# Optimization experiments

Hardware: AMD Instinct MI355X
Metric: run time of the kernel (lower is better)

## Reference

```python
import jax, jax.numpy as jnp
import numpy as np

B, N, F_IN, T_IN = 64, 307, 3, 12
HID = 128


def setup_inputs() -> dict:
    key = jax.random.key(0)
    ks = jax.random.split(key, 7)
    s = 1.0 / np.sqrt(HID)
    x = jax.random.normal(ks[0], (B, N, F_IN, T_IN), dtype=jnp.float32)
    W_ih = jax.random.uniform(ks[1], (4 * HID, F_IN), minval=-s, maxval=s, dtype=jnp.float32)
    W_hh = jax.random.uniform(ks[2], (4 * HID, HID), minval=-s, maxval=s, dtype=jnp.float32)
    b_ih = jax.random.uniform(ks[3], (4 * HID,), minval=-s, maxval=s, dtype=jnp.float32)
    b_hh = jax.random.uniform(ks[4], (4 * HID,), minval=-s, maxval=s, dtype=jnp.float32)
    W_lin = jax.random.uniform(ks[5], (1, HID), minval=-s, maxval=s, dtype=jnp.float32)
    b_lin = jax.random.uniform(ks[6], (1,), minval=-s, maxval=s, dtype=jnp.float32)
    return {"x": x, "W_ih": W_ih, "W_hh": W_hh, "b_ih": b_ih, "b_hh": b_hh, "W_lin": W_lin, "b_lin": b_lin}


def _lstm_forward(x, W_ih, W_hh, b_ih, b_hh, W_lin, b_lin):
    # x: (B, N, F_in, T_in) -> permute -> (B, N, T, F) -> reshape (B*N, T, F)
    xp = jnp.transpose(x, (0, 1, 3, 2)).reshape(B * N, T_IN, F_IN)
    # PyTorch nn.LSTM default batch_first=False: dim0 (B*N) is the time axis,
    # dim1 (T_IN) is the batch axis. We faithfully scan over B*N steps.
    # Precompute input gates for all steps: (S, Tb, 4H)
    gx = jnp.einsum('stf,gf->stg', xp, W_ih) + b_ih + b_hh
    W_hh_T = W_hh.T  # (H, 4H)

    def step(carry, g):
        h, c = carry  # (Tb, H)
        z = g + h @ W_hh_T  # (Tb, 4H)
        i, f, gg, o = jnp.split(z, 4, axis=-1)
        c = jax.nn.sigmoid(f) * c + jax.nn.sigmoid(i) * jnp.tanh(gg)
        h = jax.nn.sigmoid(o) * jnp.tanh(c)
        return (h, c), h

    h0 = jnp.zeros((T_IN, HID), dtype=x.dtype)
    _, hs = jax.lax.scan(step, (h0, h0), gx)  # hs: (S, Tb, H)
    out = hs @ W_lin.T + b_lin  # (S, Tb, 1)
    return out.reshape(B, N, T_IN)


def reference(x, W_ih, W_hh, b_ih, b_hh, W_lin, b_lin):
    return _lstm_forward(x, W_ih, W_hh, b_ih, b_hh, W_lin, b_lin)
```

## Files before the change

### kernel.cpp

```cpp
#include <hip/hip_runtime.h>

#define S_TOTAL 19648
#define T_CH    12
#define HID     128
#define NT      512

#define CHUNK_L 77
#define NCHUNK  256
#define WARMUP  32

typedef _Float16 half8  __attribute__((ext_vector_type(8)));
typedef _Float16 half4v __attribute__((ext_vector_type(4)));
typedef _Float16 half2v __attribute__((ext_vector_type(2)));
typedef float f4 __attribute__((ext_vector_type(4)));

#define NLOG2E  (-1.4426950408889634f)
#define N2LOG2E (-2.8853900817779268f)

#if __has_builtin(__builtin_amdgcn_exp2f)
#define EXP2(x) __builtin_amdgcn_exp2f(x)
#else
#define EXP2(x) __expf((x) * 0.69314718055994531f)
#endif

__device__ __forceinline__ float sigz(float z) {
    return __builtin_amdgcn_rcpf(1.0f + EXP2(z));
}
__device__ __forceinline__ float tanz(float z) {
    return __builtin_fmaf(2.0f, __builtin_amdgcn_rcpf(1.0f + EXP2(z)), -1.0f);
}
__device__ __forceinline__ float fdot2(half2v a, half2v b, float c) {
    return __builtin_amdgcn_fdot2(a, b, c, false);
}
#define MFMA(A, B, C) __builtin_amdgcn_mfma_f32_16x16x32_f16(A, B, C, 0, 0, 0)

__global__ __launch_bounds__(NT, 2) void lstm_fused(
    const float* __restrict__ x,
    const float* __restrict__ W_ih,
    const float* __restrict__ W_hh,
    const float* __restrict__ b_ih,
    const float* __restrict__ b_hh,
    const float* __restrict__ W_lin,
    const float* __restrict__ b_lin,
    float* __restrict__ out)
{
    const int tid = threadIdx.x;
    const int w   = tid >> 6;
    const int l   = tid & 63;
    const int n   = l & 15;
    const int qk  = l >> 4;

    const int ostart = blockIdx.x * CHUNK_L;
    const int oend   = min(ostart + CHUNK_L, S_TOTAL);
    const int sbeg   = max(0, ostart - WARMUP);
    const int nsteps = oend - sbeg;

    __shared__ __align__(16) _Float16 hfrag[2][5][64][8];
    __shared__ float pout[2][16][8];

    half8 A[4][5];
#pragma unroll
    for (int q = 0; q < 4; ++q) {
        const float sc = (q == 2) ? N2LOG2E : NLOG2E;
        const int row = q * HID + 16 * w + (l & 15);
#pragma unroll
        for (int kt = 0; kt < 4; ++kt) {
            const float* src = &W_hh[row * HID + kt * 32 + qk * 8];
            half8 a;
#pragma unroll
            for (int e = 0; e < 8; ++e) a[e] = (_Float16)(src[e] * sc);
            A[q][kt] = a;
        }
        half8 ae = {};
        if (qk == 0) {
            ae[0] = (_Float16)(W_ih[row * 3 + 0] * sc);
            ae[1] = (_Float16)(W_ih[row * 3 + 1] * sc);
            ae[2] = (_Float16)(W_ih[row * 3 + 2] * sc);
            ae[3] = (_Float16)((b_ih[row] + b_hh[row]) * sc);
        }
        A[q][4] = ae;
    }

    const int j0 = 16 * w + 4 * qk;
    half2v wl01, wl23;
    wl01[0] = (_Float16)W_lin[j0];     wl01[1] = (_Float16)W_lin[j0 + 1];
    wl23[0] = (_Float16)W_lin[j0 + 2]; wl23[1] = (_Float16)W_lin[j0 + 3];
    const float blin = b_lin[0];

    ((uint4*)hfrag)[tid] = make_uint4(0, 0, 0, 0);
    if (tid < 128) ((uint4*)hfrag)[512 + tid] = make_uint4(0, 0, 0, 0);
    __syncthreads();
    if (tid < 16) {
        hfrag[0][4][tid][3] = (_Float16)1.0f;
        hfrag[1][4][tid][3] = (_Float16)1.0f;
    }
    if (tid < T_CH) {
        hfrag[0][4][tid][0] = (_Float16)x[sbeg * 36 + tid];
        hfrag[0][4][tid][1] = (_Float16)x[sbeg * 36 + 12 + tid];
        hfrag[0][4][tid][2] = (_Float16)x[sbeg * 36 + 24 + tid];
    }

    const _Float16* rb0 = &hfrag[0][0][l][0];
    const _Float16* rb1 = &hfrag[1][0][l][0];
    const int ktw = w >> 1;
    const int lp  = (2 * (w & 1) + (qk >> 1)) * 16 + n;
    _Float16* wb0 = &hfrag[0][ktw][lp][4 * (qk & 1)];
    _Float16* wb1 = &hfrag[1][ktw][lp][4 * (qk & 1)];

    float c0 = 0.f, c1 = 0.f, c2 = 0.f, c3 = 0.f;

    float xn1a = 0.f, xn1b = 0.f, xn1c = 0.f;
    float xn2a = 0.f, xn2b = 0.f, xn2c = 0.f;
    if (w == 0 && l < T_CH) {
        const int s1 = min(sbeg + 1, S_TOTAL - 1);
        const int s2 = min(sbeg + 2, S_TOTAL - 1);
        xn1a = x[s1 * 36 + l]; xn1b = x[s1 * 36 + 12 + l]; xn1c = x[s1 * 36 + 24 + l];
        xn2a = x[s2 * 36 + l]; xn2b = x[s2 * 36 + 12 + l]; xn2c = x[s2 * 36 + 24 + l];
    }
    __syncthreads();

    auto step = [&](const int p, const int s) {
        const _Float16* rb = p ? rb1 : rb0;

        const half8 B0 = *(const half8*)(rb + 0 * 512);
        const half8 B1 = *(const half8*)(rb + 1 * 512);
        const half8 B2 = *(const half8*)(rb + 2 * 512);
        const half8 B3 = *(const half8*)(rb + 3 * 512);
        const half8 B4 = *(const half8*)(rb + 4 * 512);

        if (w == 7 && l < T_CH && s > ostart) {
            const f4 pa = *(const f4*)&pout[p ^ 1][l][0];
            const f4 pb = *(const f4*)&pout[p ^ 1][l][4];
            out[(s - 1) * T_CH + l] =
                pa.x + pa.y + pa.z + pa.w + pb.x + pb.y + pb.z + pb.w + blin;
        }
        if (w == 0 && l < T_CH) {
            _Float16* xd = p ? &hfrag[0][4][l][0] : &hfrag[1][4][l][0];
            half2v xp; xp[0] = (_Float16)xn1a; xp[1] = (_Float16)xn1b;
            *(half2v*)xd = xp;
            xd[2] = (_Float16)xn1c;
            xn1a = xn2a; xn1b = xn2b; xn1c = xn2c;
            const int sn = min(s + 3, S_TOTAL - 1);
            xn2a = x[sn * 36 + l];
            xn2b = x[sn * 36 + 12 + l];
            xn2c = x[sn * 36 + 24 + l];
        }

        const f4 z = {0.f, 0.f, 0.f, 0.f};
        f4 a0A = MFMA(A[0][4], B4, z), a1A = MFMA(A[1][4], B4, z);
        f4 a2A = MFMA(A[2][4], B4, z), a3A = MFMA(A[3][4], B4, z);
        f4 a0B = MFMA(A[0][2], B2, z), a1B = MFMA(A[1][2], B2, z);
        f4 a2B = MFMA(A[2][2], B2, z), a3B = MFMA(A[3][2], B2, z);
        a0A = MFMA(A[0][0], B0, a0A); a1A = MFMA(A[1][0], B0, a1A);
        a2A = MFMA(A[2][0], B0, a2A); a3A = MFMA(A[3][0], B0, a3A);
        a0B = MFMA(A[0][3], B3, a0B); a1B = MFMA(A[1][3], B3, a1B);
        a2B = MFMA(A[2][3], B3, a2B); a3B = MFMA(A[3][3], B3, a3B);
        a0A = MFMA(A[0][1], B1, a0A); a1A = MFMA(A[1][1], B1, a1A);
        a2A = MFMA(A[2][1], B1, a2A); a3A = MFMA(A[3][1], B1, a3A);
        const f4 ac0 = a0A + a0B, ac1 = a1A + a1B;
        const f4 ac2 = a2A + a2B, ac3 = a3A + a3B;

        float h0, h1, h2, h3;
        {
            const float i0 = sigz(ac0[0]), f0 = sigz(ac1[0]);
            const float g0 = tanz(ac2[0]), o0 = sigz(ac3[0]);
            c0 = __builtin_fmaf(f0, c0, i0 * g0);  h0 = o0 * tanz(c0 * N2LOG2E);
            const float i1 = sigz(ac0[1]), f1 = sigz(ac1[1]);
            const float g1 = tanz(ac2[1]), o1 = sigz(ac3[1]);
            c1 = __builtin_fmaf(f1, c1, i1 * g1);  h1 = o1 * tanz(c1 * N2LOG2E);
            const float i2 = sigz(ac0[2]), f2 = sigz(ac1[2]);
            const float g2 = tanz(ac2[2]), o2 = sigz(ac3[2]);
            c2 = __builtin_fmaf(f2, c2, i2 * g2);  h2 = o2 * tanz(c2 * N2LOG2E);
            const float i3 = sigz(ac0[3]), f3 = sigz(ac1[3]);
            const float g3 = tanz(ac2[3]), o3 = sigz(ac3[3]);
            c3 = __builtin_fmaf(f3, c3, i3 * g3);  h3 = o3 * tanz(c3 * N2LOG2E);
        }

        half4v hv;
        hv[0] = (_Float16)h0; hv[1] = (_Float16)h1;
        hv[2] = (_Float16)h2; hv[3] = (_Float16)h3;
        *(half4v*)(p ? wb0 : wb1) = hv;

        if (s >= ostart) {
            half2v hp01, hp23;
            hp01[0] = hv[0]; hp01[1] = hv[1];
            hp23[0] = hv[2]; hp23[1] = hv[3];
            float pp = fdot2(hp23, wl23, fdot2(hp01, wl01, 0.0f));
            pp += __shfl_xor(pp, 16, 64);
            pp += __shfl_xor(pp, 32, 64);
            if (qk == 0) pout[p][n][w] = pp;
        }
        __syncthreads();
    };

    int ss = 0;
    for (; ss + 2 <= nsteps; ss += 2) {
        step(0, sbeg + ss);
        step(1, sbeg + ss + 1);
    }
    if (ss < nsteps) step(0, sbeg + ss);

    if (w == 7 && l < T_CH) {
        const int pf = (nsteps - 1) & 1;
        const f4 pa = *(const f4*)&pout[pf][l][0];
        const f4 pb = *(const f4*)&pout[pf][l][4];
        out[(oend - 1) * T_CH + l] =
            pa.x + pa.y + pa.z + pa.w + pb.x + pb.y + pb.z + pb.w + blin;
    }
}

extern "C" void kernel_launch(void* const* d_in, const int* in_sizes, int n_in,
                              void* d_out, int out_size, void* d_ws, size_t ws_size,
                              hipStream_t stream) {
    const float* x     = (const float*)d_in[0];
    const float* W_ih  = (const float*)d_in[1];
    const float* W_hh  = (const float*)d_in[2];
    const float* b_ih  = (const float*)d_in[3];
    const float* b_hh  = (const float*)d_in[4];
    const float* W_lin = (const float*)d_in[5];
    const float* b_lin = (const float*)d_in[6];
    float* out = (float*)d_out;

    hipLaunchKernelGGL(lstm_fused, dim3(NCHUNK), dim3(NT), 0, stream,
                       x, W_ih, W_hh, b_ih, b_hh, W_lin, b_lin, out);
}
```

Measured before the change: 179.6 us.

## Interleave two independent sequence chunks per block to hide recurrence latency

Each block now runs two independent time chunks (A and B) of half the previous length side by side, issuing their MFMAs interleaved and sharing one barrier per step. This targets the serial dependency latency of the per-step recurrence: the B chain can fill MFMA and transcendental pipeline bubbles while the A chain waits. Halving the chunk length shortens the serial critical path, but the fixed 32-step warmup now covers a larger share of each chunk, so redundant work rises and per-thread register and LDS use roughly doubles.

```diff
diff --git a/kernel.cpp b/kernel.cpp
--- a/kernel.cpp
+++ b/kernel.cpp
@@ -5,8 +5,8 @@
 #define HID     128
 #define NT      512
 
-#define CHUNK_L 77
-#define NCHUNK  256
+#define CHUNK_L 39
+#define NBLK    252
 #define WARMUP  32
 
 typedef _Float16 half8  __attribute__((ext_vector_type(8)));
@@ -50,13 +50,17 @@
     const int n   = l & 15;
     const int qk  = l >> 4;
 
-    const int ostart = blockIdx.x * CHUNK_L;
-    const int oend   = min(ostart + CHUNK_L, S_TOTAL);
-    const int sbeg   = max(0, ostart - WARMUP);
-    const int nsteps = oend - sbeg;
-
-    __shared__ __align__(16) _Float16 hfrag[2][5][64][8];
-    __shared__ float pout[2][16][8];
+    const int cA = 2 * blockIdx.x, cB = cA + 1;
+    const int ostartA = cA * CHUNK_L, oendA = min(ostartA + CHUNK_L, S_TOTAL);
+    const int ostartB = cB * CHUNK_L, oendB = min(ostartB + CHUNK_L, S_TOTAL);
+    const int sbegA = max(0, ostartA - WARMUP);
+    const int sbegB = max(0, ostartB - WARMUP);
+    const int nstepsA = oendA - sbegA;
+    const int nstepsB = oendB - sbegB;
+    const int nsteps  = max(nstepsA, nstepsB);
+
+    __shared__ __align__(16) _Float16 hfrag[2][2][5][64][8];
+    __shared__ __align__(16) float pout[2][2][16][8];
 
     half8 A[4][5];
 #pragma unroll
@@ -87,124 +91,211 @@
     wl23[0] = (_Float16)W_lin[j0 + 2]; wl23[1] = (_Float16)W_lin[j0 + 3];
     const float blin = b_lin[0];
 
-    ((uint4*)hfrag)[tid] = make_uint4(0, 0, 0, 0);
-    if (tid < 128) ((uint4*)hfrag)[512 + tid] = make_uint4(0, 0, 0, 0);
+    uint4* hz = (uint4*)hfrag;
+    hz[tid]       = make_uint4(0, 0, 0, 0);
+    hz[tid + 512] = make_uint4(0, 0, 0, 0);
+    if (tid < 256) hz[tid + 1024] = make_uint4(0, 0, 0, 0);
     __syncthreads();
     if (tid < 16) {
-        hfrag[0][4][tid][3] = (_Float16)1.0f;
-        hfrag[1][4][tid][3] = (_Float16)1.0f;
-    }
-    if (tid < T_CH) {
-        hfrag[0][4][tid][0] = (_Float16)x[sbeg * 36 + tid];
-        hfrag[0][4][tid][1] = (_Float16)x[sbeg * 36 + 12 + tid];
-        hfrag[0][4][tid][2] = (_Float16)x[sbeg * 36 + 24 + tid];
-    }
-
-    const _Float16* rb0 = &hfrag[0][0][l][0];
-    const _Float16* rb1 = &hfrag[1][0][l][0];
+        hfrag[0][0][4][tid][3] = (_Float16)1.0f;
+        hfrag[0][1][4][tid][3] = (_Float16)1.0f;
+        hfrag[1][0][4][tid][3] = (_Float16)1.0f;
+        hfrag[1][1][4][tid][3] = (_Float16)1.0f;
+    }
+    if (w == 0 && l < T_CH) {
+        hfrag[0][0][4][l][0] = (_Float16)x[sbegA * 36 + l];
+        hfrag[0][0][4][l][1] = (_Float16)x[sbegA * 36 + 12 + l];
+        hfrag[0][0][4][l][2] = (_Float16)x[sbegA * 36 + 24 + l];
+    }
+    if (w == 1 && l < T_CH) {
+        hfrag[1][0][4][l][0] = (_Float16)x[sbegB * 36 + l];
+        hfrag[1][0][4][l][1] = (_Float16)x[sbegB * 36 + 12 + l];
+        hfrag[1][0][4][l][2] = (_Float16)x[sbegB * 36 + 24 + l];
+    }
+
+    const _Float16* rbA0 = &hfrag[0][0][0][l][0];
+    const _Float16* rbA1 = &hfrag[0][1][0][l][0];
+    const _Float16* rbB0 = &hfrag[1][0][0][l][0];
+    const _Float16* rbB1 = &hfrag[1][1][0][l][0];
     const int ktw = w >> 1;
     const int lp  = (2 * (w & 1) + (qk >> 1)) * 16 + n;
-    _Float16* wb0 = &hfrag[0][ktw][lp][4 * (qk & 1)];
-    _Float16* wb1 = &hfrag[1][ktw][lp][4 * (qk & 1)];
-
-    float c0 = 0.f, c1 = 0.f, c2 = 0.f, c3 = 0.f;
-
-    float xn1a = 0.f, xn1b = 0.f, xn1c = 0.f;
-    float xn2a = 0.f, xn2b = 0.f, xn2c = 0.f;
+    _Float16* wbA0 = &hfrag[0][0][ktw][lp][4 * (qk & 1)];
+    _Float16* wbA1 = &hfrag[0][1][ktw][lp][4 * (qk & 1)];
+    _Float16* wbB0 = &hfrag[1][0][ktw][lp][4 * (qk & 1)];
+    _Float16* wbB1 = &hfrag[1][1][ktw][lp][4 * (qk & 1)];
+
+    float cA0 = 0.f, cA1 = 0.f, cA2 = 0.f, cA3 = 0.f;
+    float cB0 = 0.f, cB1 = 0.f, cB2 = 0.f, cB3 = 0.f;
+
+    float xA1a = 0.f, xA1b = 0.f, xA1c = 0.f, xA2a = 0.f, xA2b = 0.f, xA2c = 0.f;
+    float xB1a = 0.f, xB1b = 0.f, xB1c = 0.f, xB2a = 0.f, xB2b = 0.f, xB2c = 0.f;
     if (w == 0 && l < T_CH) {
-        const int s1 = min(sbeg + 1, S_TOTAL - 1);
-        const int s2 = min(sbeg + 2, S_TOTAL - 1);
-        xn1a = x[s1 * 36 + l]; xn1b = x[s1 * 36 + 12 + l]; xn1c = x[s1 * 36 + 24 + l];
-        xn2a = x[s2 * 36 + l]; xn2b = x[s2 * 36 + 12 + l]; xn2c = x[s2 * 36 + 24 + l];
+        const int s1 = min(sbegA + 1, S_TOTAL - 1);
+        const int s2 = min(sbegA + 2, S_TOTAL - 1);
+        xA1a = x[s1 * 36 + l]; xA1b = x[s1 * 36 + 12 + l]; xA1c = x[s1 * 36 + 24 + l];
+        xA2a = x[s2 * 36 + l]; xA2b = x[s2 * 36 + 12 + l]; xA2c = x[s2 * 36 + 24 + l];
+    }
+    if (w == 1 && l < T_CH) {
+        const int s1 = min(sbegB + 1, S_TOTAL - 1);
+        const int s2 = min(sbegB + 2, S_TOTAL - 1);
+        xB1a = x[s1 * 36 + l]; xB1b = x[s1 * 36 + 12 + l]; xB1c = x[s1 * 36 + 24 + l];
+        xB2a = x[s2 * 36 + l]; xB2b = x[s2 * 36 + 12 + l]; xB2c = x[s2 * 36 + 24 + l];
     }
     __syncthreads();
 
-    auto step = [&](const int p, const int s) {
-        const _Float16* rb = p ? rb1 : rb0;
-
-        const half8 B0 = *(const half8*)(rb + 0 * 512);
-        const half8 B1 = *(const half8*)(rb + 1 * 512);
-        const half8 B2 = *(const half8*)(rb + 2 * 512);
-        const half8 B3 = *(const half8*)(rb + 3 * 512);
-        const half8 B4 = *(const half8*)(rb + 4 * 512);
-
-        if (w == 7 && l < T_CH && s > ostart) {
-            const f4 pa = *(const f4*)&pout[p ^ 1][l][0];
-            const f4 pb = *(const f4*)&pout[p ^ 1][l][4];
-            out[(s - 1) * T_CH + l] =
+    auto step = [&](const int p, const int sA, const int sB) {
+        const _Float16* ra = p ? rbA1 : rbA0;
+        const _Float16* rb = p ? rbB1 : rbB0;
+
+        const half8 BA0 = *(const half8*)(ra + 0 * 512);
+        const half8 BA1 = *(const half8*)(ra + 1 * 512);
+        const half8 BA2 = *(const half8*)(ra + 2 * 512);
+        const half8 BA3 = *(const half8*)(ra + 3 * 512);
+        const half8 BA4 = *(const half8*)(ra + 4 * 512);
+        const half8 BB0 = *(const half8*)(rb + 0 * 512);
+        const half8 BB1 = *(const half8*)(rb + 1 * 512);
+        const half8 BB2 = *(const half8*)(rb + 2 * 512);
+        const half8 BB3 = *(const half8*)(rb + 3 * 512);
+        const half8 BB4 = *(const half8*)(rb + 4 * 512);
+
+        if (w == 7 && l < T_CH && sA > ostartA && sA <= oendA) {
+            const f4 pa = *(const f4*)&pout[0][p ^ 1][l][0];
+            const f4 pb = *(const f4*)&pout[0][p ^ 1][l][4];
+            out[(sA - 1) * T_CH + l] =
                 pa.x + pa.y + pa.z + pa.w + pb.x + pb.y + pb.z + pb.w + blin;
         }
+        if (w == 6 && l < T_CH && sB > ostartB && sB <= oendB) {
+            const f4 pa = *(const f4*)&pout[1][p ^ 1][l][0];
+            const f4 pb = *(const f4*)&pout[1][p ^ 1][l][4];
+            out[(sB - 1) * T_CH + l] =
+                pa.x + pa.y + pa.z + pa.w + pb.x + pb.y + pb.z + pb.w + blin;
+        }
+
         if (w == 0 && l < T_CH) {
-            _Float16* xd = p ? &hfrag[0][4][l][0] : &hfrag[1][4][l][0];
-            half2v xp; xp[0] = (_Float16)xn1a; xp[1] = (_Float16)xn1b;
+            _Float16* xd = p ? &hfrag[0][0][4][l][0] : &hfrag[0][1][4][l][0];
+            half2v xp; xp[0] = (_Float16)xA1a; xp[1] = (_Float16)xA1b;
             *(half2v*)xd = xp;
-            xd[2] = (_Float16)xn1c;
-            xn1a = xn2a; xn1b = xn2b; xn1c = xn2c;
-            const int sn = min(s + 3, S_TOTAL - 1);
-            xn2a = x[sn * 36 + l];
-            xn2b = x[sn * 36 + 12 + l];
-            xn2c = x[sn * 36 + 24 + l];
+            xd[2] = (_Float16)xA1c;
+            xA1a = xA2a; xA1b = xA2b; xA1c = xA2c;
+            const int sn = min(sA + 3, S_TOTAL - 1);
+            xA2a = x[sn * 36 + l];
+            xA2b = x[sn * 36 + 12 + l];
+            xA2c = x[sn * 36 + 24 + l];
+        }
+        if (w == 1 && l < T_CH) {
+            _Float16* xd = p ? &hfrag[1][0][4][l][0] : &hfrag[1][1][4][l][0];
+            half2v xp; xp[0] = (_Float16)xB1a; xp[1] = (_Float16)xB1b;
+            *(half2v*)xd = xp;
+            xd[2] = (_Float16)xB1c;
+            xB1a = xB2a; xB1b = xB2b; xB1c = xB2c;
+            const int sn = min(sB + 3, S_TOTAL - 1);
+            xB2a = x[sn * 36 + l];
+            xB2b = x[sn * 36 + 12 + l];
+            xB2c = x[sn * 36 + 24 + l];
         }
 
         const f4 z = {0.f, 0.f, 0.f, 0.f};
-        f4 a0A = MFMA(A[0][4], B4, z), a1A = MFMA(A[1][4], B4, z);
-        f4 a2A = MFMA(A[2][4], B4, z), a3A = MFMA(A[3][4], B4, z);
-        f4 a0B = MFMA(A[0][2], B2, z), a1B = MFMA(A[1][2], B2, z);
-        f4 a2B = MFMA(A[2][2], B2, z), a3B = MFMA(A[3][2], B2, z);
-        a0A = MFMA(A[0][0], B0, a0A); a1A = MFMA(A[1][0], B0, a1A);
-        a2A = MFMA(A[2][0], B0, a2A); a3A = MFMA(A[3][0], B0, a3A);
-        a0B = MFMA(A[0][3], B3, a0B); a1B = MFMA(A[1][3], B3, a1B);
-        a2B = MFMA(A[2][3], B3, a2B); a3B = MFMA(A[3][3], B3, a3B);
-        a0A = MFMA(A[0][1], B1, a0A); a1A = MFMA(A[1][1], B1, a1A);
-        a2A = MFMA(A[2][1], B1, a2A); a3A = MFMA(A[3][1], B1, a3A);
-        const f4 ac0 = a0A + a0B, ac1 = a1A + a1B;
-        const f4 ac2 = a2A + a2B, ac3 = a3A + a3B;
-
-        float h0, h1, h2, h3;
+        f4 aA0 = MFMA(A[0][4], BA4, z), aB0 = MFMA(A[0][4], BB4, z);
+        f4 aA1 = MFMA(A[1][4], BA4, z), aB1 = MFMA(A[1][4], BB4, z);
+        f4 aA2 = MFMA(A[2][4], BA4, z), aB2 = MFMA(A[2][4], BB4, z);
+        f4 aA3 = MFMA(A[3][4], BA4, z), aB3 = MFMA(A[3][4], BB4, z);
+        aA0 = MFMA(A[0][0], BA0, aA0); aB0 = MFMA(A[0][0], BB0, aB0);
+        aA1 = MFMA(A[1][0], BA0, aA1); aB1 = MFMA(A[1][0], BB0, aB1);
+        aA2 = MFMA(A[2][0], BA0, aA2); aB2 = MFMA(A[2][0], BB0, aB2);
+        aA3 = MFMA(A[3][0], BA0, aA3); aB3 = MFMA(A[3][0], BB0, aB3);
+        aA0 = MFMA(A[0][1], BA1, aA0); aB0 = MFMA(A[0][1], BB1, aB0);
+        aA1 = MFMA(A[1][1], BA1, aA1); aB1 = MFMA(A[1][1], BB1, aB1);
+        aA2 = MFMA(A[2][1], BA1, aA2); aB2 = MFMA(A[2][1], BB1, aB2);
+        aA3 = MFMA(A[3][1], BA1, aA3); aB3 = MFMA(A[3][1], BB1, aB3);
+        aA0 = MFMA(A[0][2], BA2, aA0); aB0 = MFMA(A[0][2], BB2, aB0);
+        aA1 = MFMA(A[1][2], BA2, aA1); aB1 = MFMA(A[1][2], BB2, aB1);
+        aA2 = MFMA(A[2][2], BA2, aA2); aB2 = MFMA(A[2][2], BB2, aB2);
+        aA3 = MFMA(A[3][2], BA2, aA3); aB3 = MFMA(A[3][2], BB2, aB3);
+        aA0 = MFMA(A[0][3], BA3, aA0); aB0 = MFMA(A[0][3], BB3, aB0);
+        aA1 = MFMA(A[1][3], BA3, aA1); aB1 = MFMA(A[1][3], BB3, aB1);
+        aA2 = MFMA(A[2][3], BA3, aA2); aB2 = MFMA(A[2][3], BB3, aB2);
+        aA3 = MFMA(A[3][3], BA3, aA3); aB3 = MFMA(A[3][3], BB3, aB3);
+
+        float hA0, hA1, hA2, hA3;
         {
-            const float i0 = sigz(ac0[0]), f0 = sigz(ac1[0]);
-            const float g0 = tanz(ac2[0]), o0 = sigz(ac3[0]);
-            c0 = __builtin_fmaf(f0, c0, i0 * g0);  h0 = o0 * tanz(c0 * N2LOG2E);
-            const float i1 = sigz(ac0[1]), f1 = sigz(ac1[1]);
-            const float g1 = tanz(ac2[1]), o1 = sigz(ac3[1]);
-            c1 = __builtin_fmaf(f1, c1, i1 * g1);  h1 = o1 * tanz(c1 * N2LOG2E);
-            const float i2 = sigz(ac0[2]), f2 = sigz(ac1[2]);
-            const float g2 = tanz(ac2[2]), o2 = sigz(ac3[2]);
-            c2 = __builtin_fmaf(f2, c2, i2 * g2);  h2 = o2 * tanz(c2 * N2LOG2E);
-            const float i3 = sigz(ac0[3]), f3 = sigz(ac1[3]);
-            const float g3 = tanz(ac2[3]), o3 = sigz(ac3[3]);
-            c3 = __builtin_fmaf(f3, c3, i3 * g3);  h3 = o3 * tanz(c3 * N2LOG2E);
-        }
-
-        half4v hv;
-        hv[0] = (_Float16)h0; hv[1] = (_Float16)h1;
-        hv[2] = (_Float16)h2; hv[3] = (_Float16)h3;
-        *(half4v*)(p ? wb0 : wb1) = hv;
-
-        if (s >= ostart) {
-            half2v hp01, hp23;
-            hp01[0] = hv[0]; hp01[1] = hv[1];
-            hp23[0] = hv[2]; hp23[1] = hv[3];
-            float pp = fdot2(hp23, wl23, fdot2(hp01, wl01, 0.0f));
+            const float i0 = sigz(aA0[0]), f0 = sigz(aA1[0]);
+            const float g0 = tanz(aA2[0]), o0 = sigz(aA3[0]);
+            cA0 = __builtin_fmaf(f0, cA0, i0 * g0);  hA0 = o0 * tanz(cA0 * N2LOG2E);
+            const float i1 = sigz(aA0[1]), f1 = sigz(aA1[1]);
+            const float g1 = tanz(aA2[1]), o1 = sigz(aA3[1]);
+            cA1 = __builtin_fmaf(f1, cA1, i1 * g1);  hA1 = o1 * tanz(cA1 * N2LOG2E);
+            const float i2 = sigz(aA0[2]), f2 = sigz(aA1[2]);
+            const float g2 = tanz(aA2[2]), o2 = sigz(aA3[2]);
+            cA2 = __builtin_fmaf(f2, cA2, i2 * g2);  hA2 = o2 * tanz(cA2 * N2LOG2E);
+            const float i3 = sigz(aA0[3]), f3 = sigz(aA1[3]);
+            const float g3 = tanz(aA2[3]), o3 = sigz(aA3[3]);
+            cA3 = __builtin_fmaf(f3, cA3, i3 * g3);  hA3 = o3 * tanz(cA3 * N2LOG2E);
+        }
+        half4v hvA;
+        hvA[0] = (_Float16)hA0; hvA[1] = (_Float16)hA1;
+        hvA[2] = (_Float16)hA2; hvA[3] = (_Float16)hA3;
+        *(half4v*)(p ? wbA0 : wbA1) = hvA;
+
+        float hB0, hB1, hB2, hB3;
+        {
+            const float i0 = sigz(aB0[0]), f0 = sigz(aB1[0]);
+            const float g0 = tanz(aB2[0]), o0 = sigz(aB3[0]);
+            cB0 = __builtin_fmaf(f0, cB0, i0 * g0);  hB0 = o0 * tanz(cB0 * N2LOG2E);
+            const float i1 = sigz(aB0[1]), f1 = sigz(aB1[1]);
+            const float g1 = tanz(aB2[1]), o1 = sigz(aB3[1]);
+            cB1 = __builtin_fmaf(f1, cB1, i1 * g1);  hB1 = o1 * tanz(cB1 * N2LOG2E);
+            const float i2 = sigz(aB0[2]), f2 = sigz(aB1[2]);
+            const float g2 = tanz(aB2[2]), o2 = sigz(aB3[2]);
+            cB2 = __builtin_fmaf(f2, cB2, i2 * g2);  hB2 = o2 * tanz(cB2 * N2LOG2E);
+            const float i3 = sigz(aB0[3]), f3 = sigz(aB1[3]);
+            const float g3 = tanz(aB2[3]), o3 = sigz(aB3[3]);
+            cB3 = __builtin_fmaf(f3, cB3, i3 * g3);  hB3 = o3 * tanz(cB3 * N2LOG2E);
+        }
+        half4v hvB;
+        hvB[0] = (_Float16)hB0; hvB[1] = (_Float16)hB1;
+        hvB[2] = (_Float16)hB2; hvB[3] = (_Float16)hB3;
+        *(half4v*)(p ? wbB0 : wbB1) = hvB;
+
+        if (sA >= ostartA && sA < oendA) {
+            half2v h01, h23;
+            h01[0] = hvA[0]; h01[1] = hvA[1];
+            h23[0] = hvA[2]; h23[1] = hvA[3];
+            float pp = fdot2(h23, wl23, fdot2(h01, wl01, 0.0f));
             pp += __shfl_xor(pp, 16, 64);
             pp += __shfl_xor(pp, 32, 64);
-            if (qk == 0) pout[p][n][w] = pp;
+            if (qk == 0) pout[0][p][n][w] = pp;
+        }
+        if (sB >= ostartB && sB < oendB) {
+            half2v h01, h23;
+            h01[0] = hvB[0]; h01[1] = hvB[1];
+            h23[0] = hvB[2]; h23[1] = hvB[3];
+            float pp = fdot2(h23, wl23, fdot2(h01, wl01, 0.0f));
+            pp += __shfl_xor(pp, 16, 64);
+            pp += __shfl_xor(pp, 32, 64);
+            if (qk == 0) pout[1][p][n][w] = pp;
         }
         __syncthreads();
     };
 
     int ss = 0;
     for (; ss + 2 <= nsteps; ss += 2) {
-        step(0, sbeg + ss);
-        step(1, sbeg + ss + 1);
-    }
-    if (ss < nsteps) step(0, sbeg + ss);
-
-    if (w == 7 && l < T_CH) {
+        step(0, sbegA + ss, sbegB + ss);
+        step(1, sbegA + ss + 1, sbegB + ss + 1);
+    }
+    if (ss < nsteps) step(0, sbegA + ss, sbegB + ss);
+
+    if (w == 7 && l < T_CH && nstepsA == nsteps) {
         const int pf = (nsteps - 1) & 1;
-        const f4 pa = *(const f4*)&pout[pf][l][0];
-        const f4 pb = *(const f4*)&pout[pf][l][4];
-        out[(oend - 1) * T_CH + l] =
+        const f4 pa = *(const f4*)&pout[0][pf][l][0];
+        const f4 pb = *(const f4*)&pout[0][pf][l][4];
+        out[(oendA - 1) * T_CH + l] =
+            pa.x + pa.y + pa.z + pa.w + pb.x + pb.y + pb.z + pb.w + blin;
+    }
+    if (w == 6 && l < T_CH && nstepsB == nsteps) {
+        const int pf = (nsteps - 1) & 1;
+        const f4 pa = *(const f4*)&pout[1][pf][l][0];
+        const f4 pb = *(const f4*)&pout[1][pf][l][4];
+        out[(oendB - 1) * T_CH + l] =
             pa.x + pa.y + pa.z + pa.w + pb.x + pb.y + pb.z + pb.w + blin;
     }
 }
@@ -221,6 +312,6 @@
     const float* b_lin = (const float*)d_in[6];
     float* out = (float*)d_out;
 
-    hipLaunchKernelGGL(lstm_fused, dim3(NCHUNK), dim3(NT), 0, stream,
+    hipLaunchKernelGGL(lstm_fused, dim3(NBLK), dim3(NT), 0, stream,
                        x, W_ih, W_hh, b_ih, b_hh, W_lin, b_lin, out);
 }
```

After: 193.9 us. 8.0% more time.

## Interleave two independent LSTM chunk chains per block to overlap MFMA and gate math

Applied to the files above, without the earlier changes.

Each block now runs two independent sequence chunks, halving the chunk length to 39 and launching 252 blocks. The loop alternates between them: one chain's recurrent MFMAs are issued while the other chain's gate nonlinearities, output reduction and input staging run, each in its own shared-memory buffer. This targets the latency-bound serial recurrence and cuts the number of serial steps per block. In exchange, the fixed 32-step warmup is now a larger share of each shorter chunk, and register pressure rises because two accumulator and cell-state sets are live at once.

```diff
diff --git a/kernel.cpp b/kernel.cpp
--- a/kernel.cpp
+++ b/kernel.cpp
@@ -5,8 +5,8 @@
 #define HID     128
 #define NT      512
 
-#define CHUNK_L 77
-#define NCHUNK  256
+#define CHUNK_L 39
+#define NBLK    252
 #define WARMUP  32
 
 typedef _Float16 half8  __attribute__((ext_vector_type(8)));
@@ -33,6 +33,95 @@
     return __builtin_amdgcn_fdot2(a, b, c, false);
 }
 #define MFMA(A, B, C) __builtin_amdgcn_mfma_f32_16x16x32_f16(A, B, C, 0, 0, 0)
+
+#define LOADS(CIDX)                                                      \
+    {                                                                    \
+        const _Float16* rbp = &hfrag[CIDX][0][l][0];                     \
+        Bf0 = *(const half8*)(rbp + 0 * 512);                            \
+        Bf1 = *(const half8*)(rbp + 1 * 512);                            \
+        Bf2 = *(const half8*)(rbp + 2 * 512);                            \
+        Bf3 = *(const half8*)(rbp + 3 * 512);                            \
+        Bf4 = *(const half8*)(rbp + 4 * 512);                            \
+    }
+
+#define MFMAS(X)                                                         \
+    {                                                                    \
+        const f4 z = {0.f, 0.f, 0.f, 0.f};                               \
+        a##X##0 = MFMA(A[0][4], Bf4, z);                                 \
+        a##X##1 = MFMA(A[1][4], Bf4, z);                                 \
+        a##X##2 = MFMA(A[2][4], Bf4, z);                                 \
+        a##X##3 = MFMA(A[3][4], Bf4, z);                                 \
+        a##X##0 = MFMA(A[0][0], Bf0, a##X##0);                           \
+        a##X##1 = MFMA(A[1][0], Bf0, a##X##1);                           \
+        a##X##2 = MFMA(A[2][0], Bf0, a##X##2);                           \
+        a##X##3 = MFMA(A[3][0], Bf0, a##X##3);                           \
+        a##X##0 = MFMA(A[0][1], Bf1, a##X##0);                           \
+        a##X##1 = MFMA(A[1][1], Bf1, a##X##1);                           \
+        a##X##2 = MFMA(A[2][1], Bf1, a##X##2);                           \
+        a##X##3 = MFMA(A[3][1], Bf1, a##X##3);                           \
+        a##X##0 = MFMA(A[0][2], Bf2, a##X##0);                           \
+        a##X##1 = MFMA(A[1][2], Bf2, a##X##1);                           \
+        a##X##2 = MFMA(A[2][2], Bf2, a##X##2);                           \
+        a##X##3 = MFMA(A[3][2], Bf2, a##X##3);                           \
+        a##X##0 = MFMA(A[0][3], Bf3, a##X##0);                           \
+        a##X##1 = MFMA(A[1][3], Bf3, a##X##1);                           \
+        a##X##2 = MFMA(A[2][3], Bf3, a##X##2);                           \
+        a##X##3 = MFMA(A[3][3], Bf3, a##X##3);                           \
+    }
+
+#define GATES(X, CIDX, WOUT, WXP, jv)                                    \
+    {                                                                    \
+        const int sX = sbeg##X + (jv);                                   \
+        const int pj = (jv) & 1;                                         \
+        if (w == (WOUT) && l < T_CH && sX > ostart##X && sX <= oend##X) {\
+            const f4 pa = *(const f4*)&pout[CIDX][pj ^ 1][l][0];         \
+            const f4 pb = *(const f4*)&pout[CIDX][pj ^ 1][l][4];         \
+            out[(sX - 1) * T_CH + l] = pa.x + pa.y + pa.z + pa.w         \
+                + pb.x + pb.y + pb.z + pb.w + blin;                      \
+        }                                                                \
+        if (w == (WXP) && l < T_CH) {                                    \
+            _Float16* xd = &hfrag[CIDX][4][l][0];                        \
+            half2v xp; xp[0] = (_Float16)x##X##1a;                       \
+            xp[1] = (_Float16)x##X##1b;                                  \
+            *(half2v*)xd = xp;                                           \
+            xd[2] = (_Float16)x##X##1c;                                  \
+            x##X##1a = x##X##2a; x##X##1b = x##X##2b;                    \
+            x##X##1c = x##X##2c;                                         \
+            const int sn = min(sX + 3, S_TOTAL - 1);                     \
+            x##X##2a = x[sn * 36 + l];                                   \
+            x##X##2b = x[sn * 36 + 12 + l];                              \
+            x##X##2c = x[sn * 36 + 24 + l];                              \
+        }                                                                \
+        const float i0 = sigz(a##X##0[0]), f0 = sigz(a##X##1[0]);        \
+        const float g0 = tanz(a##X##2[0]), o0 = sigz(a##X##3[0]);        \
+        c##X##0 = __builtin_fmaf(f0, c##X##0, i0 * g0);                  \
+        const float h0 = o0 * tanz(c##X##0 * N2LOG2E);                   \
+        const float i1 = sigz(a##X##0[1]), f1 = sigz(a##X##1[1]);        \
+        const float g1 = tanz(a##X##2[1]), o1 = sigz(a##X##3[1]);        \
+        c##X##1 = __builtin_fmaf(f1, c##X##1, i1 * g1);                  \
+        const float h1 = o1 * tanz(c##X##1 * N2LOG2E);                   \
+        const float i2 = sigz(a##X##0[2]), f2 = sigz(a##X##1[2]);        \
+        const float g2 = tanz(a##X##2[2]), o2 = sigz(a##X##3[2]);        \
+        c##X##2 = __builtin_fmaf(f2, c##X##2, i2 * g2);                  \
+        const float h2 = o2 * tanz(c##X##2 * N2LOG2E);                   \
+        const float i3 = sigz(a##X##0[3]), f3 = sigz(a##X##1[3]);        \
+        const float g3 = tanz(a##X##2[3]), o3 = sigz(a##X##3[3]);        \
+        c##X##3 = __builtin_fmaf(f3, c##X##3, i3 * g3);                  \
+        const float h3 = o3 * tanz(c##X##3 * N2LOG2E);                   \
+        half4v hv;                                                       \
+        hv[0] = (_Float16)h0; hv[1] = (_Float16)h1;                      \
+        hv[2] = (_Float16)h2; hv[3] = (_Float16)h3;                      \
+        *(half4v*)wb##X = hv;                                            \
+        if (sX >= ostart##X && sX < oend##X) {                           \
+            half2v h01, h23;                                             \
+            h01[0] = hv[0]; h01[1] = hv[1];                              \
+            h23[0] = hv[2]; h23[1] = hv[3];                              \
+            float pp = fdot2(h23, wl23, fdot2(h01, wl01, 0.0f));         \
+            pp += __shfl_xor(pp, 16, 64);                                \
+            pp += __shfl_xor(pp, 32, 64);                                \
+            if (qk == 0) pout[CIDX][pj][n][w] = pp;                      \
+        }                                                                \
+    }
 
 __global__ __launch_bounds__(NT, 2) void lstm_fused(
     const float* __restrict__ x,
@@ -50,13 +139,17 @@
     const int n   = l & 15;
     const int qk  = l >> 4;
 
-    const int ostart = blockIdx.x * CHUNK_L;
-    const int oend   = min(ostart + CHUNK_L, S_TOTAL);
-    const int sbeg   = max(0, ostart - WARMUP);
-    const int nsteps = oend - sbeg;
+    const int cA = 2 * blockIdx.x, cB = cA + 1;
+    const int ostartA = cA * CHUNK_L, oendA = min(ostartA + CHUNK_L, S_TOTAL);
+    const int ostartB = cB * CHUNK_L, oendB = min(ostartB + CHUNK_L, S_TOTAL);
+    const int sbegA = max(0, ostartA - WARMUP);
+    const int sbegB = max(0, ostartB - WARMUP);
+    const int nstepsA = oendA - sbegA;
+    const int nstepsB = oendB - sbegB;
+    const int nsteps  = max(nstepsA, nstepsB);
 
     __shared__ __align__(16) _Float16 hfrag[2][5][64][8];
-    __shared__ float pout[2][16][8];
+    __shared__ __align__(16) float pout[2][2][16][8];
 
     half8 A[4][5];
 #pragma unroll
@@ -87,124 +180,87 @@
     wl23[0] = (_Float16)W_lin[j0 + 2]; wl23[1] = (_Float16)W_lin[j0 + 3];
     const float blin = b_lin[0];
 
-    ((uint4*)hfrag)[tid] = make_uint4(0, 0, 0, 0);
-    if (tid < 128) ((uint4*)hfrag)[512 + tid] = make_uint4(0, 0, 0, 0);
+    uint4* hz = (uint4*)hfrag;
+    hz[tid] = make_uint4(0, 0, 0, 0);
+    if (tid < 128) hz[512 + tid] = make_uint4(0, 0, 0, 0);
     __syncthreads();
     if (tid < 16) {
         hfrag[0][4][tid][3] = (_Float16)1.0f;
         hfrag[1][4][tid][3] = (_Float16)1.0f;
     }
-    if (tid < T_CH) {
-        hfrag[0][4][tid][0] = (_Float16)x[sbeg * 36 + tid];
-        hfrag[0][4][tid][1] = (_Float16)x[sbeg * 36 + 12 + tid];
-        hfrag[0][4][tid][2] = (_Float16)x[sbeg * 36 + 24 + tid];
-    }
-
-    const _Float16* rb0 = &hfrag[0][0][l][0];
-    const _Float16* rb1 = &hfrag[1][0][l][0];
+    if (w == 0 && l < T_CH) {
+        hfrag[0][4][l][0] = (_Float16)x[sbegA * 36 + l];
+        hfrag[0][4][l][1] = (_Float16)x[sbegA * 36 + 12 + l];
+        hfrag[0][4][l][2] = (_Float16)x[sbegA * 36 + 24 + l];
+    }
+    if (w == 1 && l < T_CH) {
+        hfrag[1][4][l][0] = (_Float16)x[sbegB * 36 + l];
+        hfrag[1][4][l][1] = (_Float16)x[sbegB * 36 + 12 + l];
+        hfrag[1][4][l][2] = (_Float16)x[sbegB * 36 + 24 + l];
+    }
+
     const int ktw = w >> 1;
     const int lp  = (2 * (w & 1) + (qk >> 1)) * 16 + n;
-    _Float16* wb0 = &hfrag[0][ktw][lp][4 * (qk & 1)];
-    _Float16* wb1 = &hfrag[1][ktw][lp][4 * (qk & 1)];
-
-    float c0 = 0.f, c1 = 0.f, c2 = 0.f, c3 = 0.f;
-
-    float xn1a = 0.f, xn1b = 0.f, xn1c = 0.f;
-    float xn2a = 0.f, xn2b = 0.f, xn2c = 0.f;
+    _Float16* wbA = &hfrag[0][ktw][lp][4 * (qk & 1)];
+    _Float16* wbB = &hfrag[1][ktw][lp][4 * (qk & 1)];
+
+    f4 aA0 = {0.f,0.f,0.f,0.f}, aA1 = aA0, aA2 = aA0, aA3 = aA0;
+    f4 aB0 = aA0, aB1 = aA0, aB2 = aA0, aB3 = aA0;
+    float cA0 = 0.f, cA1 = 0.f, cA2 = 0.f, cA3 = 0.f;
+    float cB0 = 0.f, cB1 = 0.f, cB2 = 0.f, cB3 = 0.f;
+
+    float xA1a = 0.f, xA1b = 0.f, xA1c = 0.f, xA2a = 0.f, xA2b = 0.f, xA2c = 0.f;
+    float xB1a = 0.f, xB1b = 0.f, xB1c = 0.f, xB2a = 0.f, xB2b = 0.f, xB2c = 0.f;
     if (w == 0 && l < T_CH) {
-        const int s1 = min(sbeg + 1, S_TOTAL - 1);
-        const int s2 = min(sbeg + 2, S_TOTAL - 1);
-        xn1a = x[s1 * 36 + l]; xn1b = x[s1 * 36 + 12 + l]; xn1c = x[s1 * 36 + 24 + l];
-        xn2a = x[s2 * 36 + l]; xn2b = x[s2 * 36 + 12 + l]; xn2c = x[s2 * 36 + 24 + l];
+        const int s1 = min(sbegA + 1, S_TOTAL - 1);
+        const int s2 = min(sbegA + 2, S_TOTAL - 1);
+        xA1a = x[s1 * 36 + l]; xA1b = x[s1 * 36 + 12 + l]; xA1c = x[s1 * 36 + 24 + l];
+        xA2a = x[s2 * 36 + l]; xA2b = x[s2 * 36 + 12 + l]; xA2c = x[s2 * 36 + 24 + l];
+    }
+    if (w == 1 && l < T_CH) {
+        const int s1 = min(sbegB + 1, S_TOTAL - 1);
+        const int s2 = min(sbegB + 2, S_TOTAL - 1);
+        xB1a = x[s1 * 36 + l]; xB1b = x[s1 * 36 + 12 + l]; xB1c = x[s1 * 36 + 24 + l];
+        xB2a = x[s2 * 36 + l]; xB2b = x[s2 * 36 + 12 + l]; xB2c = x[s2 * 36 + 24 + l];
     }
     __syncthreads();
 
-    auto step = [&](const int p, const int s) {
-        const _Float16* rb = p ? rb1 : rb0;
-
-        const half8 B0 = *(const half8*)(rb + 0 * 512);
-        const half8 B1 = *(const half8*)(rb + 1 * 512);
-        const half8 B2 = *(const half8*)(rb + 2 * 512);
-        const half8 B3 = *(const half8*)(rb + 3 * 512);
-        const half8 B4 = *(const half8*)(rb + 4 * 512);
-
-        if (w == 7 && l < T_CH && s > ostart) {
-            const f4 pa = *(const f4*)&pout[p ^ 1][l][0];
-            const f4 pb = *(const f4*)&pout[p ^ 1][l][4];
-            out[(s - 1) * T_CH + l] =
-                pa.x + pa.y + pa.z + pa.w + pb.x + pb.y + pb.z + pb.w + blin;
-        }
-        if (w == 0 && l < T_CH) {
-            _Float16* xd = p ? &hfrag[0][4][l][0] : &hfrag[1][4][l][0];
-            half2v xp; xp[0] = (_Float16)xn1a; xp[1] = (_Float16)xn1b;
-            *(half2v*)xd = xp;
-            xd[2] = (_Float16)xn1c;
-            xn1a = xn2a; xn1b = xn2b; xn1c = xn2c;
-            const int sn = min(s + 3, S_TOTAL - 1);
-            xn2a = x[sn * 36 + l];
-            xn2b = x[sn * 36 + 12 + l];
-            xn2c = x[sn * 36 + 24 + l];
-        }
-
-        const f4 z = {0.f, 0.f, 0.f, 0.f};
-        f4 a0A = MFMA(A[0][4], B4, z), a1A = MFMA(A[1][4], B4, z);
-        f4 a2A = MFMA(A[2][4], B4, z), a3A = MFMA(A[3][4], B4, z);
-        f4 a0B = MFMA(A[0][2], B2, z), a1B = MFMA(A[1][2], B2, z);
-        f4 a2B = MFMA(A[2][2], B2, z), a3B = MFMA(A[3][2], B2, z);
-        a0A = MFMA(A[0][0], B0, a0A); a1A = MFMA(A[1][0], B0, a1A);
-        a2A = MFMA(A[2][0], B0, a2A); a3A = MFMA(A[3][0], B0, a3A);
-        a0B = MFMA(A[0][3], B3, a0B); a1B = MFMA(A[1][3], B3, a1B);
-        a2B = MFMA(A[2][3], B3, a2B); a3B = MFMA(A[3][3], B3, a3B);
-        a0A = MFMA(A[0][1], B1, a0A); a1A = MFMA(A[1][1], B1, a1A);
-        a2A = MFMA(A[2][1], B1, a2A); a3A = MFMA(A[3][1], B1, a3A);
-        const f4 ac0 = a0A + a0B, ac1 = a1A + a1B;
-        const f4 ac2 = a2A + a2B, ac3 = a3A + a3B;
-
-        float h0, h1, h2, h3;
+    {
+        half8 Bf0, Bf1, Bf2, Bf3, Bf4;
+        LOADS(0);
+        MFMAS(A);
+    }
+    __syncthreads();
+
+    for (int i = 0; i < nsteps; ++i) {
         {
-            const float i0 = sigz(ac0[0]), f0 = sigz(ac1[0]);
-            const float g0 = tanz(ac2[0]), o0 = sigz(ac3[0]);
-            c0 = __builtin_fmaf(f0, c0, i0 * g0);  h0 = o0 * tanz(c0 * N2LOG2E);
-            const float i1 = sigz(ac0[1]), f1 = sigz(ac1[1]);
-            const float g1 = tanz(ac2[1]), o1 = sigz(ac3[1]);
-            c1 = __builtin_fmaf(f1, c1, i1 * g1);  h1 = o1 * tanz(c1 * N2LOG2E);
-            const float i2 = sigz(ac0[2]), f2 = sigz(ac1[2]);
-            const float g2 = tanz(ac2[2]), o2 = sigz(ac3[2]);
-            c2 = __builtin_fmaf(f2, c2, i2 * g2);  h2 = o2 * tanz(c2 * N2LOG2E);
-            const float i3 = sigz(ac0[3]), f3 = sigz(ac1[3]);
-            const float g3 = tanz(ac2[3]), o3 = sigz(ac3[3]);
-            c3 = __builtin_fmaf(f3, c3, i3 * g3);  h3 = o3 * tanz(c3 * N2LOG2E);
-        }
-
-        half4v hv;
-        hv[0] = (_Float16)h0; hv[1] = (_Float16)h1;
-        hv[2] = (_Float16)h2; hv[3] = (_Float16)h3;
-        *(half4v*)(p ? wb0 : wb1) = hv;
-
-        if (s >= ostart) {
-            half2v hp01, hp23;
-            hp01[0] = hv[0]; hp01[1] = hv[1];
-            hp23[0] = hv[2]; hp23[1] = hv[3];
-            float pp = fdot2(hp23, wl23, fdot2(hp01, wl01, 0.0f));
-            pp += __shfl_xor(pp, 16, 64);
-            pp += __shfl_xor(pp, 32, 64);
-            if (qk == 0) pout[p][n][w] = pp;
+            half8 Bf0, Bf1, Bf2, Bf3, Bf4;
+            LOADS(1);
+            GATES(A, 0, 7, 0, i);
+            MFMAS(B);
         }
         __syncthreads();
-    };
-
-    int ss = 0;
-    for (; ss + 2 <= nsteps; ss += 2) {
-        step(0, sbeg + ss);
-        step(1, sbeg + ss + 1);
-    }
-    if (ss < nsteps) step(0, sbeg + ss);
-
-    if (w == 7 && l < T_CH) {
-        const int pf = (nsteps - 1) & 1;
-        const f4 pa = *(const f4*)&pout[pf][l][0];
-        const f4 pb = *(const f4*)&pout[pf][l][4];
-        out[(oend - 1) * T_CH + l] =
+        {
+            half8 Bf0, Bf1, Bf2, Bf3, Bf4;
+            LOADS(0);
+            GATES(B, 1, 6, 1, i);
+            MFMAS(A);
+        }
+        __syncthreads();
+    }
+
+    if (w == 7 && l < T_CH && nstepsA == nsteps) {
+        const int pf = (nstepsA - 1) & 1;
+        const f4 pa = *(const f4*)&pout[0][pf][l][0];
+        const f4 pb = *(const f4*)&pout[0][pf][l][4];
+        out[(oendA - 1) * T_CH + l] =
+            pa.x + pa.y + pa.z + pa.w + pb.x + pb.y + pb.z + pb.w + blin;
+    }
+    if (w == 6 && l < T_CH && nstepsB == nsteps) {
+        const int pf = (nstepsB - 1) & 1;
+        const f4 pa = *(const f4*)&pout[1][pf][l][0];
+        const f4 pb = *(const f4*)&pout[1][pf][l][4];
+        out[(oendB - 1) * T_CH + l] =
             pa.x + pa.y + pa.z + pa.w + pb.x + pb.y + pb.z + pb.w + blin;
     }
 }
@@ -221,6 +277,6 @@
     const float* b_lin = (const float*)d_in[6];
     float* out = (float*)d_out;
 
-    hipLaunchKernelGGL(lstm_fused, dim3(NCHUNK), dim3(NT), 0, stream,
+    hipLaunchKernelGGL(lstm_fused, dim3(NBLK), dim3(NT), 0, stream,
                        x, W_ih, W_hh, b_ih, b_hh, W_lin, b_lin, out);
 }
```

Result: slower. 188.5 us (+5.0%).
